# Optimization experiments

Hardware: AMD Instinct MI355X
Metric: run time of the kernel (lower is better)

## Reference

```python
import jax, jax.numpy as jnp
import numpy as np

B, C, N, D, S = 512, 256, 2048, 64, 3

def setup_inputs() -> dict:
    key = jax.random.key(0)
    k1, k2, k3, k4, k5 = jax.random.split(key, 5)
    controller_output = jax.random.normal(k1, (B, C), dtype=jnp.float32)
    w_prev = jax.random.uniform(k2, (B, N), dtype=jnp.float32)
    w_prev = w_prev / jnp.sum(w_prev, axis=-1, keepdims=True)  # valid attention weighting
    M_t = jax.random.normal(k3, (B, N, D), dtype=jnp.float32)
    emit_len = D + 1 + 1 + S + 1  # read_split sum = 70
    W = jax.random.normal(k4, (C, emit_len), dtype=jnp.float32) * (1.0 / np.sqrt(C))
    b = jax.random.normal(k5, (emit_len,), dtype=jnp.float32) * 0.05
    return {"controller_output": controller_output, "w_t_1": w_prev, "M_t": M_t, "W": W, "b": b}

def reference(controller_output, w_t_1, M_t, W, b):
    # fc_addr: Dense with tanh activation
    fc = jnp.tanh(controller_output @ W + b)  # [B, 70]
    # split per read_split [D,1,1,S,1] and apply emit activations
    k_t = fc[:, :D]                                            # [B, D] (already tanh'd)
    beta_t = jax.nn.softplus(fc[:, D:D + 1])                   # [B, 1] key strength
    g_t = jax.nn.sigmoid(fc[:, D + 1:D + 2])                   # [B, 1] interpolation gate
    s_t = jax.nn.softmax(fc[:, D + 2:D + 2 + S], axis=-1)      # [B, S] shift weighting
    gamma_t = 1.0 + jax.nn.softplus(fc[:, D + 2 + S:D + 3 + S])  # [B, 1] sharpen
    # content addressing: cosine similarity (no epsilon, faithful to source)
    dot = jnp.einsum('bd,bnd->bn', k_t, M_t)                   # [B, N]
    k_mag = jnp.sqrt(jnp.sum(k_t * k_t, axis=-1, keepdims=True))  # [B, 1]
    m_mag = jnp.sqrt(jnp.sum(M_t * M_t, axis=-1))              # [B, N]
    cos = dot / (k_mag * m_mag)
    w_c_t = jax.nn.softmax(beta_t * cos, axis=-1)              # [B, N]
    # interpolation
    w_g_t = g_t * w_c_t + (1.0 - g_t) * w_t_1                  # [B, N]
    # circular convolution shift: sum_i roll(w, i - S//2) * s[:, i]
    w_tilde = jnp.zeros_like(w_g_t)
    for i in range(S):
        w_tilde = w_tilde + jnp.roll(w_g_t, i - S // 2, axis=-1) * s_t[:, i:i + 1]
    # sharpening
    w_raised = jnp.power(w_tilde, gamma_t)
    w_t = w_raised / jnp.sum(w_raised, axis=-1, keepdims=True)  # [B, N]
    # read
    r_t = jnp.einsum('bn,bnd->bd', w_t, M_t)                   # [B, D]
    return (r_t, w_t)
```

## Files before the change

kernel.cpp:

```cpp
#include <hip/hip_runtime.h>
#include <math.h>

constexpr int Bb = 512;
constexpr int Cc = 256;
constexpr int Nn = 2048;
constexpr int Dd = 64;
constexpr int EMIT = Dd + 1 + 1 + 3 + 1;
constexpr int BLOCK = 512;
constexpr int NW = BLOCK / 64;

__global__ __launch_bounds__(BLOCK, 4)
void ntm_read_head_kernel(const float* __restrict__ co,
                          const float* __restrict__ wprev,
                          const float* __restrict__ M,
                          const float* __restrict__ W,
                          const float* __restrict__ bias,
                          float* __restrict__ out_r,
                          float* __restrict__ out_w)
{
    const int b    = blockIdx.x;
    const int t    = threadIdx.x;
    const int lane = t & 63;
    const int wv   = t >> 6;

    __shared__ __align__(16) float fc[EMIT + 2];
    __shared__ float sc[8];
    __shared__ float zbuf[Nn];
    __shared__ float wgbuf[Nn];
    __shared__ float wtbuf[Nn];
    __shared__ float red[NW];
    __shared__ float rred[NW][Dd];

    const float* corow = co + (size_t)b * Cc;
    if (t < EMIT * 4) {
        const int j = t >> 2, p = t & 3;
        float s = 0.f;
        const float* wp = W + j;
        #pragma unroll 8
        for (int c = p * 64; c < p * 64 + 64; ++c)
            s += corow[c] * wp[(size_t)c * EMIT];
        s += __shfl_xor(s, 1);
        s += __shfl_xor(s, 2);
        if (p == 0) fc[j] = tanhf(s + bias[j]);
    }
    __syncthreads();

    if (t < 64) {
        float kk  = fc[t];
        float ksq = kk * kk;
        #pragma unroll
        for (int o = 1; o < 64; o <<= 1) ksq += __shfl_xor(ksq, o);
        if (t == 0) {
            float kmag  = sqrtf(ksq);
            float beta  = log1pf(expf(fc[Dd]));
            float g     = 1.f / (1.f + expf(-fc[Dd + 1]));
            float f0 = fc[Dd + 2], f1 = fc[Dd + 3], f2 = fc[Dd + 4];
            float mx = fmaxf(f0, fmaxf(f1, f2));
            float e0 = expf(f0 - mx), e1 = expf(f1 - mx), e2 = expf(f2 - mx);
            float ei = 1.f / (e0 + e1 + e2);
            float gamma = 1.f + log1pf(expf(fc[Dd + 5]));
            sc[0] = beta; sc[1] = g;
            sc[2] = e0 * ei; sc[3] = e1 * ei; sc[4] = e2 * ei;
            sc[5] = gamma; sc[6] = 1.f / kmag;
        }
    }
    __syncthreads();

    const size_t mbase = (size_t)b * Nn * Dd;
    const int grp = t >> 4;
    const int dk  = t & 15;
    {
        const float beta = sc[0];
        const float kinv = sc[6];
        const float4 kf = *(const float4*)&fc[dk * 4];
        for (int n = grp; n < Nn; n += BLOCK / 16) {
            const float4 m = *(const float4*)&M[mbase + (size_t)n * Dd + dk * 4];
            float dot = kf.x * m.x + kf.y * m.y + kf.z * m.z + kf.w * m.w;
            float msq = m.x * m.x + m.y * m.y + m.z * m.z + m.w * m.w;
            #pragma unroll
            for (int o = 1; o < 16; o <<= 1) {
                dot += __shfl_xor(dot, o);
                msq += __shfl_xor(msq, o);
            }
            if (dk == 0) zbuf[n] = beta * dot * kinv / sqrtf(msq);
        }
    }
    __syncthreads();

    float lm = -3.4e38f;
    for (int n = t; n < Nn; n += BLOCK) lm = fmaxf(lm, zbuf[n]);
    #pragma unroll
    for (int o = 1; o < 64; o <<= 1) lm = fmaxf(lm, __shfl_xor(lm, o));
    if (lane == 0) red[wv] = lm;
    __syncthreads();
    float zmax = red[0];
    #pragma unroll
    for (int w = 1; w < NW; ++w) zmax = fmaxf(zmax, red[w]);
    __syncthreads();

    float ls = 0.f;
    for (int n = t; n < Nn; n += BLOCK) {
        float e = expf(zbuf[n] - zmax);
        zbuf[n] = e;
        ls += e;
    }
    #pragma unroll
    for (int o = 1; o < 64; o <<= 1) ls += __shfl_xor(ls, o);
    if (lane == 0) red[wv] = ls;
    __syncthreads();
    float Zs = 0.f;
    #pragma unroll
    for (int w = 0; w < NW; ++w) Zs += red[w];

    {
        const float g = sc[1];
        const float invZ = 1.f / Zs;
        const float* wpv = wprev + (size_t)b * Nn;
        for (int n = t; n < Nn; n += BLOCK)
            wgbuf[n] = g * zbuf[n] * invZ + (1.f - g) * wpv[n];
    }
    __syncthreads();

    float lsum = 0.f;
    {
        const float s0 = sc[2], s1 = sc[3], s2 = sc[4], gamma = sc[5];
        for (int n = t; n < Nn; n += BLOCK) {
            float wt_ = s0 * wgbuf[(n + 1) & (Nn - 1)]
                      + s1 * wgbuf[n]
                      + s2 * wgbuf[(n - 1) & (Nn - 1)];
            float wr = powf(wt_, gamma);
            wtbuf[n] = wr;
            lsum += wr;
        }
    }
    #pragma unroll
    for (int o = 1; o < 64; o <<= 1) lsum += __shfl_xor(lsum, o);
    if (lane == 0) red[wv] = lsum;
    __syncthreads();
    float Ws = 0.f;
    #pragma unroll
    for (int w = 0; w < NW; ++w) Ws += red[w];

    {
        const float inv = 1.f / Ws;
        float* ow = out_w + (size_t)b * Nn;
        for (int n = t; n < Nn; n += BLOCK) {
            float v = wtbuf[n] * inv;
            wtbuf[n] = v;
            ow[n] = v;
        }
    }
    __syncthreads();

    {
        float4 acc = make_float4(0.f, 0.f, 0.f, 0.f);
        for (int n = grp; n < Nn; n += BLOCK / 16) {
            const float w = wtbuf[n];
            const float4 m = *(const float4*)&M[mbase + (size_t)n * Dd + dk * 4];
            acc.x += w * m.x; acc.y += w * m.y;
            acc.z += w * m.z; acc.w += w * m.w;
        }
        #pragma unroll
        for (int o = 16; o < 64; o <<= 1) {
            acc.x += __shfl_xor(acc.x, o);
            acc.y += __shfl_xor(acc.y, o);
            acc.z += __shfl_xor(acc.z, o);
            acc.w += __shfl_xor(acc.w, o);
        }
        if (lane < 16) {
            rred[wv][lane * 4 + 0] = acc.x;
            rred[wv][lane * 4 + 1] = acc.y;
            rred[wv][lane * 4 + 2] = acc.z;
            rred[wv][lane * 4 + 3] = acc.w;
        }
    }
    __syncthreads();
    if (t < Dd) {
        float r = 0.f;
        #pragma unroll
        for (int w = 0; w < NW; ++w) r += rred[w][t];
        out_r[(size_t)b * Dd + t] = r;
    }
}

extern "C" void kernel_launch(void* const* d_in, const int* in_sizes, int n_in,
                              void* d_out, int out_size, void* d_ws, size_t ws_size,
                              hipStream_t stream) {
    const float* co    = (const float*)d_in[0];
    const float* wprev = (const float*)d_in[1];
    const float* M     = (const float*)d_in[2];
    const float* W     = (const float*)d_in[3];
    const float* bias  = (const float*)d_in[4];
    float* out = (float*)d_out;
    float* out_r = out;
    float* out_w = out + (size_t)Bb * Dd;

    ntm_read_head_kernel<<<Bb, BLOCK, 0, stream>>>(co, wprev, M, W, bias, out_r, out_w);
}
```

Baseline: 100.5 us.

## Double block size, split FC GEMV across threads, 4 lanes per memory row

Raises the block to 1024 threads. The controller GEMV is recomputed with 980 threads, each summing a 19-element chunk of C; partial sums are staged in zbuf and then reduced by 70 threads. The cosine pass now gives each 4-thread group one full memory row of 16 floats per thread, cutting the shuffle reduction from 4 levels to 2 and issuing more loads per thread. The read pass gets unroll 2. The larger block means fewer blocks resident per CU and more register pressure, and the FC weight loads are no longer coalesced across the C dimension.

```diff
diff --git a/kernel.cpp b/kernel.cpp
--- a/kernel.cpp
+++ b/kernel.cpp
@@ -6,10 +6,10 @@
 constexpr int Nn = 2048;
 constexpr int Dd = 64;
 constexpr int EMIT = Dd + 1 + 1 + 3 + 1;
-constexpr int BLOCK = 512;
+constexpr int BLOCK = 1024;
 constexpr int NW = BLOCK / 64;
 
-__global__ __launch_bounds__(BLOCK, 4)
+__global__ __launch_bounds__(BLOCK, 8)
 void ntm_read_head_kernel(const float* __restrict__ co,
                           const float* __restrict__ wprev,
                           const float* __restrict__ M,
@@ -25,23 +25,32 @@
 
     __shared__ __align__(16) float fc[EMIT + 2];
     __shared__ float sc[8];
-    __shared__ float zbuf[Nn];
+    __shared__ __align__(16) float zbuf[Nn];
     __shared__ float wgbuf[Nn];
     __shared__ float wtbuf[Nn];
     __shared__ float red[NW];
     __shared__ float rred[NW][Dd];
 
     const float* corow = co + (size_t)b * Cc;
-    if (t < EMIT * 4) {
-        const int j = t >> 2, p = t & 3;
-        float s = 0.f;
-        const float* wp = W + j;
-        #pragma unroll 8
-        for (int c = p * 64; c < p * 64 + 64; ++c)
-            s += corow[c] * wp[(size_t)c * EMIT];
-        s += __shfl_xor(s, 1);
-        s += __shfl_xor(s, 2);
-        if (p == 0) fc[j] = tanhf(s + bias[j]);
+    {
+        float* fcp = zbuf;
+        if (t < 980) {
+            const int j    = t % EMIT;
+            const int part = t / EMIT;
+            const int c0 = part * 19;
+            const int c1 = (c0 + 19 < Cc) ? c0 + 19 : Cc;
+            float s = 0.f;
+            for (int c = c0; c < c1; ++c)
+                s = fmaf(corow[c], W[(size_t)c * EMIT + j], s);
+            fcp[part * EMIT + j] = s;
+        }
+        __syncthreads();
+        if (t < EMIT) {
+            float s = bias[t];
+            #pragma unroll
+            for (int w = 0; w < 14; ++w) s += fcp[w * EMIT + t];
+            fc[t] = tanhf(s);
+        }
     }
     __syncthreads();
 
@@ -67,22 +76,35 @@
     __syncthreads();
 
     const size_t mbase = (size_t)b * Nn * Dd;
-    const int grp = t >> 4;
-    const int dk  = t & 15;
-    {
+    {
+        const int rg = t >> 2;
+        const int p  = t & 3;
         const float beta = sc[0];
         const float kinv = sc[6];
-        const float4 kf = *(const float4*)&fc[dk * 4];
-        for (int n = grp; n < Nn; n += BLOCK / 16) {
-            const float4 m = *(const float4*)&M[mbase + (size_t)n * Dd + dk * 4];
-            float dot = kf.x * m.x + kf.y * m.y + kf.z * m.z + kf.w * m.w;
-            float msq = m.x * m.x + m.y * m.y + m.z * m.z + m.w * m.w;
-            #pragma unroll
-            for (int o = 1; o < 16; o <<= 1) {
-                dot += __shfl_xor(dot, o);
-                msq += __shfl_xor(msq, o);
-            }
-            if (dk == 0) zbuf[n] = beta * dot * kinv / sqrtf(msq);
+        const float4 k0 = *(const float4*)&fc[p * 16 + 0];
+        const float4 k1 = *(const float4*)&fc[p * 16 + 4];
+        const float4 k2 = *(const float4*)&fc[p * 16 + 8];
+        const float4 k3 = *(const float4*)&fc[p * 16 + 12];
+        for (int n0 = 0; n0 < Nn; n0 += BLOCK / 4) {
+            const int n = n0 + rg;
+            const float4* mr = (const float4*)&M[mbase + (size_t)n * Dd + p * 16];
+            const float4 m0 = mr[0];
+            const float4 m1 = mr[1];
+            const float4 m2 = mr[2];
+            const float4 m3 = mr[3];
+            float dot = m0.x*k0.x + m0.y*k0.y + m0.z*k0.z + m0.w*k0.w
+                      + m1.x*k1.x + m1.y*k1.y + m1.z*k1.z + m1.w*k1.w
+                      + m2.x*k2.x + m2.y*k2.y + m2.z*k2.z + m2.w*k2.w
+                      + m3.x*k3.x + m3.y*k3.y + m3.z*k3.z + m3.w*k3.w;
+            float msq = m0.x*m0.x + m0.y*m0.y + m0.z*m0.z + m0.w*m0.w
+                      + m1.x*m1.x + m1.y*m1.y + m1.z*m1.z + m1.w*m1.w
+                      + m2.x*m2.x + m2.y*m2.y + m2.z*m2.z + m2.w*m2.w
+                      + m3.x*m3.x + m3.y*m3.y + m3.z*m3.z + m3.w*m3.w;
+            dot += __shfl_xor(dot, 1);
+            msq += __shfl_xor(msq, 1);
+            dot += __shfl_xor(dot, 2);
+            msq += __shfl_xor(msq, 2);
+            if (p == 0) zbuf[n] = beta * dot * kinv / sqrtf(msq);
         }
     }
     __syncthreads();
@@ -153,7 +175,10 @@
     __syncthreads();
 
     {
+        const int grp = t >> 4;
+        const int dk  = t & 15;
         float4 acc = make_float4(0.f, 0.f, 0.f, 0.f);
+        #pragma unroll 2
         for (int n = grp; n < Nn; n += BLOCK / 16) {
             const float w = wtbuf[n];
             const float4 m = *(const float4*)&M[mbase + (size_t)n * Dd + dk * 4];
```

New measurement: 88.37 us. 1.14x faster.
